# Kernel optimization log

Hardware: AMD Instinct MI355X
Metric: run time of the kernel (lower is better)

## Reference

```python
import jax, jax.numpy as jnp
import numpy as np

EPS = 1e-7
INF = 1e8
NUM_CLASSES = 80
SOFT_CENTER_RADIUS = 3.0
TOPK = 13
IOU_WEIGHT = 3.0

B, N, G, C = 16, 8400, 100, NUM_CLASSES
IMG = 640.0


def setup_inputs() -> dict:
    key = jax.random.key(0)
    ks = jax.random.split(key, 8)
    # anchor priors: centers in image, stride column (cx, cy, s, s)
    ctr = jax.random.uniform(ks[0], (N, 2)) * IMG
    stride = jnp.full((N, 1), 8.0)
    priors = jnp.concatenate([ctr, stride, stride], axis=-1)
    # predicted boxes: xyxy around random centers
    pc = jax.random.uniform(ks[1], (B, N, 2)) * IMG
    pwh = jax.random.uniform(ks[2], (B, N, 2)) * 64.0 + 8.0
    pred_bboxes = jnp.concatenate([pc - pwh / 2, pc + pwh / 2], axis=-1)
    pred_scores = jax.random.normal(ks[3], (B, N, C))
    # gt boxes: xyxy
    gc = jax.random.uniform(ks[4], (B, G, 2)) * (IMG - 40.0) + 20.0
    gwh = jax.random.uniform(ks[5], (B, G, 2)) * 128.0 + 16.0
    gt_bboxes = jnp.concatenate([gc - gwh / 2, gc + gwh / 2], axis=-1)
    gt_labels = jax.random.randint(ks[6], (B, G, 1), 0, NUM_CLASSES, dtype=jnp.int32)
    pad_bbox_flag = jnp.ones((B, G, 1), dtype=jnp.float32)
    gt_bboxes_area = gwh[..., 0] * gwh[..., 1]
    area_rule = jnp.array([0.0, 32.0, 96.0, 1.0e4], dtype=jnp.float32)
    return {
        'pred_bboxes': pred_bboxes, 'pred_scores': pred_scores, 'priors': priors,
        'gt_labels': gt_labels, 'gt_bboxes': gt_bboxes, 'pad_bbox_flag': pad_bbox_flag,
        'gt_bboxes_area': gt_bboxes_area, 'area_rule': area_rule,
    }


def _giou(b1, b2):
    # b1, b2 broadcastable [..., 4] xyxy -> GIoU [...]
    lt = jnp.maximum(b1[..., :2], b2[..., :2])
    rb = jnp.minimum(b1[..., 2:], b2[..., 2:])
    wh = jnp.clip(rb - lt, 0.0)
    overlap = wh[..., 0] * wh[..., 1]
    a1 = (b1[..., 2] - b1[..., 0]) * (b1[..., 3] - b1[..., 1])
    a2 = (b2[..., 2] - b2[..., 0]) * (b2[..., 3] - b2[..., 1])
    union = jnp.maximum(a1 + a2 - overlap, EPS)
    iou = overlap / union
    elt = jnp.minimum(b1[..., :2], b2[..., :2])
    erb = jnp.maximum(b1[..., 2:], b2[..., 2:])
    ewh = jnp.clip(erb - elt, 0.0)
    enclose = jnp.maximum(ewh[..., 0] * ewh[..., 1], EPS)
    return iou - (enclose - union) / enclose


def _forward(pred_bboxes, pred_scores, priors, gt_labels, gt_bboxes, pad_bbox_flag,
             gt_bboxes_area, area_rule):
    b, n, _ = pred_bboxes.shape
    g = gt_bboxes.shape[1]
    pts = priors[:, :2]                      # (N,2)
    # point-in-box test -> (B,N,G)
    lt = pts[None, :, None, :] - gt_bboxes[:, None, :, :2]
    rb = gt_bboxes[:, None, :, 2:] - pts[None, :, None, :]
    deltas = jnp.concatenate([lt, rb], axis=-1)          # (B,N,G,4)
    is_in = (jnp.min(deltas, axis=-1) > 0).astype(pred_bboxes.dtype)
    is_in = is_in * pad_bbox_flag[:, None, :, 0]
    # soft center prior
    gt_ctr = (gt_bboxes[..., :2] + gt_bboxes[..., 2:]) / 2.0
    strides = priors[:, 2]
    dist = jnp.sqrt(((pts[None, :, None, :] - gt_ctr[:, None, :, :]) ** 2).sum(-1))
    dist = dist / strides[None, :, None] * is_in
    soft_center_prior = jnp.power(10.0, dist - SOFT_CENTER_RADIUS) * is_in
    # pairwise GIoU (B,N,G)
    giou = _giou(pred_bboxes[:, :, None, :], gt_bboxes[:, None, :, :])
    pairwise_ious = jnp.abs(giou * is_in)
    iou_cost = -jnp.log(pairwise_ious + EPS) * IOU_WEIGHT
    # per-gt-class logit gather: (B,N,G)
    labels = gt_labels[..., 0].astype(jnp.int32)         # (B,G)
    idx = jnp.broadcast_to(labels[:, None, :], (b, n, g))
    logits = jnp.take_along_axis(pred_scores, idx, axis=2)
    sig = jax.nn.sigmoid(logits)
    scale = pairwise_ious - sig
    # stable BCE-with-logits against soft target pairwise_ious
    bce = jnp.maximum(logits, 0.0) - logits * pairwise_ious + jnp.log1p(jnp.exp(-jnp.abs(logits)))
    cls_cost = bce * jnp.exp(jnp.abs(scale) - 1.0) * jnp.abs(scale)
    cost = cls_cost + iou_cost + soft_center_prior
    in_mask = is_in > 0
    cost = jnp.where(in_mask, cost, INF)
    # dynamic-k matching
    k = min(TOPK, n)
    topk_ious = jax.lax.top_k(jnp.transpose(pairwise_ious, (0, 2, 1)), k)[0]  # (B,G,k)
    dyn_k = jnp.clip(topk_ious.sum(-1).astype(jnp.int32), 1, None)            # (B,G)
    ranks = jnp.argsort(jnp.argsort(cost, axis=1), axis=1)                    # (B,N,G)
    valid_gt = pad_bbox_flag[..., 0] > 0                                      # (B,G)
    matching = (ranks < dyn_k[:, None, :]) & valid_gt[:, None, :]             # (B,N,G)
    # resolve anchors matched to >1 gt: keep min-cost gt
    multi = matching.sum(-1) > 1                                              # (B,N)
    onehot_min = jax.nn.one_hot(jnp.argmin(cost, axis=-1), g, dtype=jnp.bool_)
    matching = jnp.where(multi[..., None], onehot_min, matching)
    fg_mask = matching.sum(-1) > 0                                            # (B,N)
    mf = matching.astype(pairwise_ious.dtype)
    matched_ious = (mf * pairwise_ious).sum(-1)                               # (B,N)
    matched_gt = jnp.argmax(mf, axis=-1)                                      # (B,N)
    # dense assignments
    assigned_labels = jnp.where(fg_mask, jnp.take_along_axis(labels, matched_gt, axis=1), NUM_CLASSES)
    gidx = jnp.broadcast_to(matched_gt[..., None], (b, n, 4))
    assigned_bboxes = jnp.where(fg_mask[..., None], jnp.take_along_axis(gt_bboxes, gidx, axis=1), 0.0)
    assign_metrics = jnp.where(fg_mask, matched_ious, 0.0)
    onehot = jax.nn.one_hot(assigned_labels, NUM_CLASSES + 1, dtype=pred_scores.dtype)[..., :NUM_CLASSES]
    assigned_scores = onehot * jnp.where(fg_mask, matched_ious, 1.0)[..., None]
    # per-class positive counts and dynamic class weights
    assigned_labels_num = (onehot * fg_mask[..., None].astype(onehot.dtype)).sum((0, 1))
    maxc = assigned_labels_num.max()
    dynamic_gt_class_weight = jnp.where(assigned_labels_num > 0,
                                        maxc / jnp.maximum(assigned_labels_num, 1.0), 1.0)
    assigned_labels_weights = jnp.where(fg_mask[..., None],
                                        dynamic_gt_class_weight[None, None, :],
                                        jnp.ones((), pred_scores.dtype))
    # gt area distribution (len(area_rule)-1, B, G)
    r2 = area_rule ** 2
    ga = gt_bboxes_area[None]
    area_dist = (ga >= r2[:-1, None, None]) & (ga < r2[1:, None, None]) & valid_gt[None]
    return (assigned_labels.astype(jnp.int32), assigned_labels_weights, assigned_bboxes,
            assigned_scores, assign_metrics, fg_mask, assigned_labels_num,
            dynamic_gt_class_weight, area_dist)


def reference(pred_bboxes, pred_scores, priors, gt_labels, gt_bboxes, pad_bbox_flag,
              gt_bboxes_area, area_rule):
    return _forward(pred_bboxes, pred_scores, priors, gt_labels, gt_bboxes,
                    pad_bbox_flag, gt_bboxes_area, area_rule)
```

## Files before the change

kernel.cpp:

```cpp
#include <hip/hip_runtime.h>

typedef unsigned long long u64;

#define BB 16
#define NN 8400
#define GG 100
#define CC 80
#define KTOP 13
#define EPSF 1e-7f
#define INFC 1e8f
#define MAXIN 1024

static constexpr size_t kO_LAB  = 0;
static constexpr size_t kO_W    = (size_t)BB * NN;
static constexpr size_t kO_BB   = kO_W + (size_t)BB * NN * CC;
static constexpr size_t kO_SC   = kO_BB + (size_t)BB * NN * 4;
static constexpr size_t kO_MET  = kO_SC + (size_t)BB * NN * CC;
static constexpr size_t kO_FG   = kO_MET + (size_t)BB * NN;
static constexpr size_t kO_NUM  = kO_FG + (size_t)BB * NN;
static constexpr size_t kO_DYNW = kO_NUM + CC;
static constexpr size_t kO_AREA = kO_DYNW + CC;

__device__ __forceinline__ unsigned f2u(float x) {
    unsigned b = __float_as_uint(x);
    return (b & 0x80000000u) ? ~b : (b | 0x80000000u);
}
__device__ __forceinline__ float u2f(unsigned e) {
    return __uint_as_float((e & 0x80000000u) ? (e & 0x7fffffffu) : ~e);
}

__device__ __forceinline__ void pair_cost_iou_inside(
    float px, float py, float st,
    float p0, float p1, float p2, float p3,
    float g0, float g1, float g2, float g3,
    float lg, float flag,
    float& cost, float& piou)
{
    float gcx = (g0 + g2) * 0.5f, gcy = (g1 + g3) * 0.5f;
    float dx = px - gcx, dy = py - gcy;
    float dist = sqrtf(dx * dx + dy * dy) / st * flag;
    float scp = exp2f((dist - 3.0f) * 3.32192809488736f) * flag;
    float ix1 = fmaxf(p0, g0), iy1 = fmaxf(p1, g1);
    float ix2 = fminf(p2, g2), iy2 = fminf(p3, g3);
    float ow = fmaxf(ix2 - ix1, 0.0f), oh = fmaxf(iy2 - iy1, 0.0f);
    float ov = ow * oh;
    float a1 = (p2 - p0) * (p3 - p1);
    float a2 = (g2 - g0) * (g3 - g1);
    float uni = fmaxf(a1 + a2 - ov, EPSF);
    float iou = ov / uni;
    float ex1 = fminf(p0, g0), ey1 = fminf(p1, g1);
    float ex2 = fmaxf(p2, g2), ey2 = fmaxf(p3, g3);
    float ew = fmaxf(ex2 - ex1, 0.0f), eh = fmaxf(ey2 - ey1, 0.0f);
    float enc = fmaxf(ew * eh, EPSF);
    float giou = iou - (enc - uni) / enc;
    piou = fabsf(giou * flag);
    float iou_cost = -__logf(piou + EPSF) * 3.0f;
    float sig = 1.0f / (1.0f + __expf(-lg));
    float sc = piou - sig;
    float asc = fabsf(sc);
    float bce = fmaxf(lg, 0.0f) - lg * piou + log1pf(__expf(-fabsf(lg)));
    float cls = bce * __expf(asc - 1.0f) * asc;
    cost = cls + iou_cost + scp;
}

__device__ __forceinline__ void pair_cost_iou(
    float px, float py, float st,
    float p0, float p1, float p2, float p3,
    float g0, float g1, float g2, float g3,
    float lg, float flag,
    float& cost, float& piou)
{
    float l = px - g0, t = py - g1, r = g2 - px, d = g3 - py;
    float mn = fminf(fminf(l, t), fminf(r, d));
    float is_in = (mn > 0.0f) ? flag : 0.0f;
    float gcx = (g0 + g2) * 0.5f, gcy = (g1 + g3) * 0.5f;
    float dx = px - gcx, dy = py - gcy;
    float dist = sqrtf(dx * dx + dy * dy) / st * is_in;
    float scp = exp2f((dist - 3.0f) * 3.32192809488736f) * is_in;
    float ix1 = fmaxf(p0, g0), iy1 = fmaxf(p1, g1);
    float ix2 = fminf(p2, g2), iy2 = fminf(p3, g3);
    float ow = fmaxf(ix2 - ix1, 0.0f), oh = fmaxf(iy2 - iy1, 0.0f);
    float ov = ow * oh;
    float a1 = (p2 - p0) * (p3 - p1);
    float a2 = (g2 - g0) * (g3 - g1);
    float uni = fmaxf(a1 + a2 - ov, EPSF);
    float iou = ov / uni;
    float ex1 = fminf(p0, g0), ey1 = fminf(p1, g1);
    float ex2 = fmaxf(p2, g2), ey2 = fmaxf(p3, g3);
    float ew = fmaxf(ex2 - ex1, 0.0f), eh = fmaxf(ey2 - ey1, 0.0f);
    float enc = fmaxf(ew * eh, EPSF);
    float giou = iou - (enc - uni) / enc;
    piou = fabsf(giou * is_in);
    float iou_cost = -__logf(piou + EPSF) * 3.0f;
    float sig = 1.0f / (1.0f + __expf(-lg));
    float sc = piou - sig;
    float asc = fabsf(sc);
    float bce = fmaxf(lg, 0.0f) - lg * piou + log1pf(__expf(-fabsf(lg)));
    float cls = bce * __expf(asc - 1.0f) * asc;
    float cc = cls + iou_cost + scp;
    cost = (is_in > 0.0f) ? cc : INFC;
}

__global__ __launch_bounds__(256) void k1_match(
    const float* __restrict__ pred_bboxes,
    const float* __restrict__ pred_scores,
    const float* __restrict__ priors,
    const int*   __restrict__ gt_labels,
    const float* __restrict__ gt_bboxes,
    const float* __restrict__ pad_flag,
    int*   __restrict__ match_count,
    int*   __restrict__ match_g,
    float* __restrict__ match_iou)
{
    __shared__ int   s_cnt;
    __shared__ int   s_list[MAXIN];
    __shared__ u64   s_cand[4 * KTOP];
    __shared__ float s_candP[4 * KTOP];
    __shared__ int   s_dynk;

    int bg = blockIdx.x;
    int b = bg / GG, g = bg - b * GG;
    int tid  = threadIdx.x;
    int lane = tid & 63;
    int w    = tid >> 6;

    float flag = pad_flag[bg];
    if (flag == 0.0f) return;

    if (tid == 0) s_cnt = 0;
    __syncthreads();

    float4 gb = *reinterpret_cast<const float4*>(gt_bboxes + (size_t)bg * 4);

    #pragma unroll 4
    for (int k = 0; k < 32; ++k) {
        int n = tid + (k << 8);
        float4 p = *reinterpret_cast<const float4*>(priors + (size_t)n * 4);
        float mn = fminf(fminf(p.x - gb.x, p.y - gb.y),
                         fminf(gb.z - p.x, gb.w - p.y));
        if (mn > 0.0f) {
            int po = atomicAdd(&s_cnt, 1);
            if (po < MAXIN) s_list[po] = n;
        }
    }
    if (tid < NN - 8192) {
        int n = tid + 8192;
        float4 p = *reinterpret_cast<const float4*>(priors + (size_t)n * 4);
        float mn = fminf(fminf(p.x - gb.x, p.y - gb.y),
                         fminf(gb.z - p.x, gb.w - p.y));
        if (mn > 0.0f) {
            int po = atomicAdd(&s_cnt, 1);
            if (po < MAXIN) s_list[po] = n;
        }
    }
    __syncthreads();
    int M = min(s_cnt, MAXIN);

    if (M == 0) {
        if (tid == 0) {
            int idx = b * NN;
            atomicAdd(&match_count[idx], 1);
            match_g[idx]   = g;
            match_iou[idx] = 0.0f;
        }
        return;
    }

    int lab = gt_labels[bg];

    u64 zs = ((u64)0x80000000u << 32) | (0x10000u + (unsigned)tid * 4u);
    u64 iK0 = zs, iK1 = zs + 1, iK2 = zs + 2, iK3 = zs + 3;
    u64 cK0 = ~0ull, cK1 = ~0ull, cK2 = ~0ull, cK3 = ~0ull;
    float cP0 = 0.f, cP1 = 0.f, cP2 = 0.f, cP3 = 0.f;

    for (int m = tid; m < M; m += 256) {
        int n = s_list[m];
        float4 pr = *reinterpret_cast<const float4*>(priors + (size_t)n * 4);
        float4 pb = *reinterpret_cast<const float4*>(pred_bboxes + ((size_t)b * NN + n) * 4);
        float lg = pred_scores[((size_t)b * NN + n) * CC + lab];
        float cost, piou;
        pair_cost_iou_inside(pr.x, pr.y, pr.z, pb.x, pb.y, pb.z, pb.w,
                             gb.x, gb.y, gb.z, gb.w, lg, flag, cost, piou);
        u64 ki = ((u64)f2u(piou) << 32) | (unsigned)n;
        if (ki > iK3) {
            iK3 = ki;
            if (iK3 > iK2) { u64 t0 = iK2; iK2 = iK3; iK3 = t0; }
            if (iK2 > iK1) { u64 t0 = iK1; iK1 = iK2; iK2 = t0; }
            if (iK1 > iK0) { u64 t0 = iK0; iK0 = iK1; iK1 = t0; }
        }
        u64 kc = ((u64)f2u(cost) << 32) | (unsigned)n;
        if (kc < cK3) {
            cK3 = kc; cP3 = piou;
            if (cK3 < cK2) { u64 t0 = cK2; cK2 = cK3; cK3 = t0; float f0 = cP2; cP2 = cP3; cP3 = f0; }
            if (cK2 < cK1) { u64 t0 = cK1; cK1 = cK2; cK2 = t0; float f0 = cP1; cP1 = cP2; cP2 = f0; }
            if (cK1 < cK0) { u64 t0 = cK0; cK0 = cK1; cK1 = t0; float f0 = cP0; cP0 = cP1; cP1 = f0; }
        }
    }

    for (int r = 0; r < KTOP; ++r) {
        u64 h = iK0;
        #pragma unroll
        for (int off = 1; off < 64; off <<= 1) {
            u64 o = __shfl_xor(h, off, 64);
            if (o > h) h = o;
        }
        if (lane == 0) s_cand[w * KTOP + r] = h;
        if (iK0 == h) { iK0 = iK1; iK1 = iK2; iK2 = iK3; iK3 = 0ull; }
    }
    __syncthreads();
    if (w == 0) {
        u64 kk = (lane < 4 * KTOP) ? s_cand[lane] : 0ull;
        float ks = 0.0f;
        for (int r = 0; r < KTOP; ++r) {
            u64 h = kk;
            #pragma unroll
            for (int off = 1; off < 64; off <<= 1) {
                u64 o = __shfl_xor(h, off, 64);
                if (o > h) h = o;
            }
            ks += u2f((unsigned)(h >> 32));
            if (kk == h) kk = 0ull;
        }
        if (lane == 0) { int dk = (int)ks; s_dynk = (dk < 1) ? 1 : dk; }
    }
    __syncthreads();
    int dyn_k = s_dynk;

    for (int r = 0; r < dyn_k; ++r) {
        u64 h = cK0;
        #pragma unroll
        for (int off = 1; off < 64; off <<= 1) {
            u64 o = __shfl_xor(h, off, 64);
            if (o < h) h = o;
        }
        if (cK0 == h) {
            s_cand[w * KTOP + r]  = h;
            s_candP[w * KTOP + r] = cP0;
            cK0 = cK1; cP0 = cP1; cK1 = cK2; cP1 = cP2; cK2 = cK3; cP2 = cP3;
            cK3 = ~0ull;
        }
    }
    __syncthreads();
    if (w == 0) {
        int tot = 4 * dyn_k;
        u64 kk = ~0ull; float pp = 0.0f;
        if (lane < tot) {
            int wv = lane / dyn_k;
            int r  = lane - wv * dyn_k;
            kk = s_cand[wv * KTOP + r];
            pp = s_candP[wv * KTOP + r];
        }
        for (int r = 0; r < dyn_k; ++r) {
            u64 h = kk;
            #pragma unroll
            for (int off = 1; off < 64; off <<= 1) {
                u64 o = __shfl_xor(h, off, 64);
                if (o < h) h = o;
            }
            if (kk == h && h != ~0ull) {
                int bi = (int)(h & 0xffffffffu);
                int idx = b * NN + bi;
                atomicAdd(&match_count[idx], 1);
                match_g[idx]   = g;
                match_iou[idx] = pp;
                kk = ~0ull;
            }
        }
    }
}

__global__ __launch_bounds__(256) void k2_resolve(
    const float* __restrict__ pred_bboxes,
    const float* __restrict__ pred_scores,
    const float* __restrict__ priors,
    const int*   __restrict__ gt_labels,
    const float* __restrict__ gt_bboxes,
    const float* __restrict__ pad_flag,
    const int*   __restrict__ match_count,
    const int*   __restrict__ match_g,
    const float* __restrict__ match_iou,
    int*   __restrict__ r_lab,
    float* __restrict__ r_miou,
    int*   __restrict__ class_num,
    float* __restrict__ out)
{
    int i = blockIdx.x * 256 + threadIdx.x;
    int lane = threadIdx.x & 63;
    int cnt = match_count[i];
    int b = i / NN;

    int lab = CC;
    float miou = 0.0f;
    float4 bbx = make_float4(0.0f, 0.0f, 0.0f, 0.0f);

    if (cnt == 1) {
        int g = match_g[i];
        int gi = b * GG + g;
        miou = match_iou[i];
        lab = gt_labels[gi];
        bbx = *reinterpret_cast<const float4*>(gt_bboxes + (size_t)gi * 4);
    }

    u64 mask = __ballot(cnt > 1);
    while (mask) {
        int src = __builtin_ctzll(mask);
        mask &= mask - 1;
        int ii = (i & ~63) | src;
        int b2 = ii / NN, n2 = ii - b2 * NN;
        float4 pr = *reinterpret_cast<const float4*>(priors + (size_t)n2 * 4);
        float4 pb = *reinterpret_cast<const float4*>(pred_bboxes + (size_t)ii * 4);
        u64 bk = ~0ull; float bp = 0.0f;
        #pragma unroll
        for (int s = 0; s < 2; ++s) {
            int gg = lane + (s << 6);
            if (gg < GG) {
                int gi = b2 * GG + gg;
                float fl = pad_flag[gi];
                float4 gbx = *reinterpret_cast<const float4*>(gt_bboxes + (size_t)gi * 4);
                int lb = gt_labels[gi];
                float lg = pred_scores[(size_t)ii * CC + lb];
                float cost, piou;
                pair_cost_iou(pr.x, pr.y, pr.z, pb.x, pb.y, pb.z, pb.w,
                              gbx.x, gbx.y, gbx.z, gbx.w, lg, fl, cost, piou);
                u64 k = ((u64)f2u(cost) << 32) | (unsigned)gg;
                if (k < bk) { bk = k; bp = piou; }
            }
        }
        #pragma unroll
        for (int off = 1; off < 64; off <<= 1) {
            u64 ok = __shfl_xor(bk, off, 64);
            float op = __shfl_xor(bp, off, 64);
            if (ok < bk) { bk = ok; bp = op; }
        }
        if (lane == src) {
            int gw = (int)(bk & 0xffffffffu);
            int gi = b2 * GG + gw;
            lab = gt_labels[gi];
            miou = bp;
            bbx = *reinterpret_cast<const float4*>(gt_bboxes + (size_t)gi * 4);
        }
    }

    bool fg = cnt > 0;
    if (fg) atomicAdd(&class_num[lab], 1);
    r_lab[i]  = lab;
    r_miou[i] = miou;
    out[kO_LAB + i] = (float)lab;
    out[kO_FG  + i] = fg ? 1.0f : 0.0f;
    out[kO_MET + i] = miou;
    *reinterpret_cast<float4*>(out + kO_BB + (size_t)i * 4) = bbx;
}

__global__ __launch_bounds__(256) void k35_weights_area(
    const int*   __restrict__ class_num,
    float* __restrict__ dynw,
    const float* __restrict__ gt_area,
    const float* __restrict__ area_rule,
    const float* __restrict__ pad_flag,
    float* __restrict__ out)
{
    if (blockIdx.x == 0) {
        int lane = threadIdx.x;
        if (lane < 64) {
            int n0 = class_num[lane];
            int n1 = (lane < CC - 64) ? class_num[lane + 64] : 0;
            int m = max(n0, n1);
            #pragma unroll
            for (int off = 32; off > 0; off >>= 1) m = max(m, __shfl_down(m, off, 64));
            m = __shfl(m, 0, 64);
            float fm = (float)m;
            {
                float wv = (n0 > 0) ? fm / fmaxf((float)n0, 1.0f) : 1.0f;
                dynw[lane] = wv;
                out[kO_NUM  + lane] = (float)n0;
                out[kO_DYNW + lane] = wv;
            }
            if (lane < CC - 64) {
                float wv = (n1 > 0) ? fm / fmaxf((float)n1, 1.0f) : 1.0f;
                dynw[lane + 64] = wv;
                out[kO_NUM  + lane + 64] = (float)n1;
                out[kO_DYNW + lane + 64] = wv;
            }
        }
    } else {
        int idx = (blockIdx.x - 1) * 256 + threadIdx.x;
        if (idx < 3 * BB * GG) {
            int z = idx / (BB * GG);
            int rem = idx - z * (BB * GG);
            float ga = gt_area[rem];
            float lo = area_rule[z] * area_rule[z];
            float hi = area_rule[z + 1] * area_rule[z + 1];
            bool v = (ga >= lo) && (ga < hi) && (pad_flag[rem] > 0.0f);
            out[kO_AREA + idx] = v ? 1.0f : 0.0f;
        }
    }
}

__global__ __launch_bounds__(256) void k4_fill(
    const int*   __restrict__ r_lab,
    const float* __restrict__ r_miou,
    const float* __restrict__ dynw,
    float* __restrict__ out)
{
    __shared__ float s_w[CC];
    if (threadIdx.x < CC) s_w[threadIdx.x] = dynw[threadIdx.x];
    __syncthreads();
    unsigned t = blockIdx.x * 256u + threadIdx.x;
    unsigned i = t / 20u;
    unsigned cq = (t - i * 20u) * 4u;
    int lab = r_lab[i];
    float miou = r_miou[i];
    bool fg = lab < CC;
    unsigned ulab = (unsigned)lab;
    float4 sc, wv;
    sc.x = (ulab == cq + 0u) ? miou : 0.0f;
    sc.y = (ulab == cq + 1u) ? miou : 0.0f;
    sc.z = (ulab == cq + 2u) ? miou : 0.0f;
    sc.w = (ulab == cq + 3u) ? miou : 0.0f;
    wv.x = fg ? s_w[cq + 0u] : 1.0f;
    wv.y = fg ? s_w[cq + 1u] : 1.0f;
    wv.z = fg ? s_w[cq + 2u] : 1.0f;
    wv.w = fg ? s_w[cq + 3u] : 1.0f;
    size_t base = (size_t)i * CC + cq;
    *reinterpret_cast<float4*>(out + kO_SC + base) = sc;
    *reinterpret_cast<float4*>(out + kO_W  + base) = wv;
}

extern "C" void kernel_launch(void* const* d_in, const int* in_sizes, int n_in,
                              void* d_out, int out_size, void* d_ws, size_t ws_size,
                              hipStream_t stream)
{
    const float* pred_bboxes = (const float*)d_in[0];
    const float* pred_scores = (const float*)d_in[1];
    const float* priors      = (const float*)d_in[2];
    const int*   gt_labels   = (const int*)d_in[3];
    const float* gt_bboxes   = (const float*)d_in[4];
    const float* pad_flag    = (const float*)d_in[5];
    const float* gt_area     = (const float*)d_in[6];
    const float* area_rule   = (const float*)d_in[7];
    float* out = (float*)d_out;

    char* w = (char*)d_ws;
    int*   match_count = (int*)w;   w += (size_t)BB * NN * 4;
    int*   class_num   = (int*)w;   w += (size_t)CC * 4;
    int*   match_g     = (int*)w;   w += (size_t)BB * NN * 4;
    float* match_iou   = (float*)w; w += (size_t)BB * NN * 4;
    int*   r_lab       = (int*)w;   w += (size_t)BB * NN * 4;
    float* r_miou      = (float*)w; w += (size_t)BB * NN * 4;
    float* dynw        = (float*)w; w += (size_t)CC * 4;

    hipMemsetAsync(d_ws, 0, (size_t)(BB * NN + CC) * 4, stream);

    k1_match<<<BB * GG, 256, 0, stream>>>(
        pred_bboxes, pred_scores, priors, gt_labels, gt_bboxes, pad_flag,
        match_count, match_g, match_iou);

    k2_resolve<<<BB * NN / 256, 256, 0, stream>>>(
        pred_bboxes, pred_scores, priors, gt_labels, gt_bboxes, pad_flag,
        match_count, match_g, match_iou, r_lab, r_miou, class_num, out);

    k35_weights_area<<<1 + (3 * BB * GG + 255) / 256, 256, 0, stream>>>(
        class_num, dynw, gt_area, area_rule, pad_flag, out);

    k4_fill<<<(int)((size_t)BB * NN * (CC / 4) / 256), 256, 0, stream>>>(
        r_lab, r_miou, dynw, out);
}
```

Measured before the change: 232.2 us.

## Replace per-thread top-k lists with shared-memory rank counting; fuse weight kernel into fill

The matching kernel no longer keeps per-thread top-4 registers merged by wavefront shuffle reductions. It stores the iou and cost keys for every candidate in shared memory and computes each candidate's rank by an O(M^2) comparison scan. That rank then gives the top-13 IoU sum and the dynamic-k selection without serial shuffle rounds. The separate class-weight/area kernel is folded into the fill kernel, with every block recomputing the 80 class weights, which removes one launch and the dynw round trip. The risks are quadratic shared-memory work when M is large and larger shared-memory use (about 18KB) lowering occupancy.

```diff
diff --git a/kernel.cpp b/kernel.cpp
--- a/kernel.cpp
+++ b/kernel.cpp
@@ -114,20 +114,20 @@
 {
     __shared__ int   s_cnt;
     __shared__ int   s_list[MAXIN];
-    __shared__ u64   s_cand[4 * KTOP];
-    __shared__ float s_candP[4 * KTOP];
-    __shared__ int   s_dynk;
+    __shared__ u64   s_kiou[MAXIN];
+    __shared__ u64   s_kcost[MAXIN];
+    __shared__ unsigned short s_rc[MAXIN];
+    __shared__ float s_top[KTOP];
 
     int bg = blockIdx.x;
     int b = bg / GG, g = bg - b * GG;
-    int tid  = threadIdx.x;
-    int lane = tid & 63;
-    int w    = tid >> 6;
+    int tid = threadIdx.x;
 
     float flag = pad_flag[bg];
     if (flag == 0.0f) return;
 
     if (tid == 0) s_cnt = 0;
+    if (tid < KTOP) s_top[tid] = 0.0f;
     __syncthreads();
 
     float4 gb = *reinterpret_cast<const float4*>(gt_bboxes + (size_t)bg * 4);
@@ -168,11 +168,6 @@
 
     int lab = gt_labels[bg];
 
-    u64 zs = ((u64)0x80000000u << 32) | (0x10000u + (unsigned)tid * 4u);
-    u64 iK0 = zs, iK1 = zs + 1, iK2 = zs + 2, iK3 = zs + 3;
-    u64 cK0 = ~0ull, cK1 = ~0ull, cK2 = ~0ull, cK3 = ~0ull;
-    float cP0 = 0.f, cP1 = 0.f, cP2 = 0.f, cP3 = 0.f;
-
     for (int m = tid; m < M; m += 256) {
         int n = s_list[m];
         float4 pr = *reinterpret_cast<const float4*>(priors + (size_t)n * 4);
@@ -181,90 +176,39 @@
         float cost, piou;
         pair_cost_iou_inside(pr.x, pr.y, pr.z, pb.x, pb.y, pb.z, pb.w,
                              gb.x, gb.y, gb.z, gb.w, lg, flag, cost, piou);
-        u64 ki = ((u64)f2u(piou) << 32) | (unsigned)n;
-        if (ki > iK3) {
-            iK3 = ki;
-            if (iK3 > iK2) { u64 t0 = iK2; iK2 = iK3; iK3 = t0; }
-            if (iK2 > iK1) { u64 t0 = iK1; iK1 = iK2; iK2 = t0; }
-            if (iK1 > iK0) { u64 t0 = iK0; iK0 = iK1; iK1 = t0; }
-        }
-        u64 kc = ((u64)f2u(cost) << 32) | (unsigned)n;
-        if (kc < cK3) {
-            cK3 = kc; cP3 = piou;
-            if (cK3 < cK2) { u64 t0 = cK2; cK2 = cK3; cK3 = t0; float f0 = cP2; cP2 = cP3; cP3 = f0; }
-            if (cK2 < cK1) { u64 t0 = cK1; cK1 = cK2; cK2 = t0; float f0 = cP1; cP1 = cP2; cP2 = f0; }
-            if (cK1 < cK0) { u64 t0 = cK0; cK0 = cK1; cK1 = t0; float f0 = cP0; cP0 = cP1; cP1 = f0; }
-        }
-    }
-
-    for (int r = 0; r < KTOP; ++r) {
-        u64 h = iK0;
-        #pragma unroll
-        for (int off = 1; off < 64; off <<= 1) {
-            u64 o = __shfl_xor(h, off, 64);
-            if (o > h) h = o;
-        }
-        if (lane == 0) s_cand[w * KTOP + r] = h;
-        if (iK0 == h) { iK0 = iK1; iK1 = iK2; iK2 = iK3; iK3 = 0ull; }
-    }
-    __syncthreads();
-    if (w == 0) {
-        u64 kk = (lane < 4 * KTOP) ? s_cand[lane] : 0ull;
-        float ks = 0.0f;
-        for (int r = 0; r < KTOP; ++r) {
-            u64 h = kk;
-            #pragma unroll
-            for (int off = 1; off < 64; off <<= 1) {
-                u64 o = __shfl_xor(h, off, 64);
-                if (o > h) h = o;
-            }
-            ks += u2f((unsigned)(h >> 32));
-            if (kk == h) kk = 0ull;
-        }
-        if (lane == 0) { int dk = (int)ks; s_dynk = (dk < 1) ? 1 : dk; }
-    }
-    __syncthreads();
-    int dyn_k = s_dynk;
-
-    for (int r = 0; r < dyn_k; ++r) {
-        u64 h = cK0;
-        #pragma unroll
-        for (int off = 1; off < 64; off <<= 1) {
-            u64 o = __shfl_xor(h, off, 64);
-            if (o < h) h = o;
-        }
-        if (cK0 == h) {
-            s_cand[w * KTOP + r]  = h;
-            s_candP[w * KTOP + r] = cP0;
-            cK0 = cK1; cP0 = cP1; cK1 = cK2; cP1 = cP2; cK2 = cK3; cP2 = cP3;
-            cK3 = ~0ull;
-        }
-    }
-    __syncthreads();
-    if (w == 0) {
-        int tot = 4 * dyn_k;
-        u64 kk = ~0ull; float pp = 0.0f;
-        if (lane < tot) {
-            int wv = lane / dyn_k;
-            int r  = lane - wv * dyn_k;
-            kk = s_cand[wv * KTOP + r];
-            pp = s_candP[wv * KTOP + r];
-        }
-        for (int r = 0; r < dyn_k; ++r) {
-            u64 h = kk;
-            #pragma unroll
-            for (int off = 1; off < 64; off <<= 1) {
-                u64 o = __shfl_xor(h, off, 64);
-                if (o < h) h = o;
-            }
-            if (kk == h && h != ~0ull) {
-                int bi = (int)(h & 0xffffffffu);
-                int idx = b * NN + bi;
-                atomicAdd(&match_count[idx], 1);
-                match_g[idx]   = g;
-                match_iou[idx] = pp;
-                kk = ~0ull;
-            }
+        s_kiou[m]  = ((u64)f2u(piou) << 32) | (unsigned)n;
+        s_kcost[m] = ((u64)f2u(cost) << 32) | (unsigned)n;
+    }
+    __syncthreads();
+
+    for (int m = tid; m < M; m += 256) {
+        u64 ki = s_kiou[m];
+        u64 kc = s_kcost[m];
+        int riou = 0, rcost = 0;
+        #pragma unroll 4
+        for (int i = 0; i < M; ++i) {
+            riou  += (s_kiou[i]  > ki) ? 1 : 0;
+            rcost += (s_kcost[i] < kc) ? 1 : 0;
+        }
+        if (riou < KTOP) s_top[riou] = u2f((unsigned)(ki >> 32));
+        s_rc[m] = (unsigned short)rcost;
+    }
+    __syncthreads();
+
+    float ksum = 0.0f;
+    #pragma unroll
+    for (int r = 0; r < KTOP; ++r) ksum += s_top[r];
+    int dyn_k = (int)ksum;
+    if (dyn_k < 1) dyn_k = 1;
+
+    for (int m = tid; m < M; m += 256) {
+        if ((int)s_rc[m] < dyn_k) {
+            u64 ki = s_kiou[m];
+            int n = (int)(ki & 0xffffffffu);
+            int idx = b * NN + n;
+            atomicAdd(&match_count[idx], 1);
+            match_g[idx]   = g;
+            match_iou[idx] = u2f((unsigned)(ki >> 32));
         }
     }
 }
@@ -351,39 +295,55 @@
     *reinterpret_cast<float4*>(out + kO_BB + (size_t)i * 4) = bbx;
 }
 
-__global__ __launch_bounds__(256) void k35_weights_area(
+#define K4MAIN ((BB * NN * (CC / 4)) / 256)
+__global__ __launch_bounds__(256) void k4_fill(
+    const int*   __restrict__ r_lab,
+    const float* __restrict__ r_miou,
     const int*   __restrict__ class_num,
-    float* __restrict__ dynw,
     const float* __restrict__ gt_area,
     const float* __restrict__ area_rule,
     const float* __restrict__ pad_flag,
     float* __restrict__ out)
 {
-    if (blockIdx.x == 0) {
-        int lane = threadIdx.x;
-        if (lane < 64) {
-            int n0 = class_num[lane];
-            int n1 = (lane < CC - 64) ? class_num[lane + 64] : 0;
-            int m = max(n0, n1);
-            #pragma unroll
-            for (int off = 32; off > 0; off >>= 1) m = max(m, __shfl_down(m, off, 64));
-            m = __shfl(m, 0, 64);
-            float fm = (float)m;
-            {
-                float wv = (n0 > 0) ? fm / fmaxf((float)n0, 1.0f) : 1.0f;
-                dynw[lane] = wv;
-                out[kO_NUM  + lane] = (float)n0;
-                out[kO_DYNW + lane] = wv;
-            }
-            if (lane < CC - 64) {
-                float wv = (n1 > 0) ? fm / fmaxf((float)n1, 1.0f) : 1.0f;
-                dynw[lane + 64] = wv;
-                out[kO_NUM  + lane + 64] = (float)n1;
-                out[kO_DYNW + lane + 64] = wv;
-            }
-        }
+    __shared__ float s_w[CC];
+    int t0 = threadIdx.x;
+    if (t0 < 64) {
+        int n0 = class_num[t0];
+        int n1 = (t0 < CC - 64) ? class_num[t0 + 64] : 0;
+        int m = max(n0, n1);
+        #pragma unroll
+        for (int off = 32; off > 0; off >>= 1) m = max(m, __shfl_down(m, off, 64));
+        m = __shfl(m, 0, 64);
+        float fm = (float)m;
+        s_w[t0] = (n0 > 0) ? fm / fmaxf((float)n0, 1.0f) : 1.0f;
+        if (t0 < CC - 64)
+            s_w[t0 + 64] = (n1 > 0) ? fm / fmaxf((float)n1, 1.0f) : 1.0f;
+    }
+    __syncthreads();
+
+    unsigned bid = blockIdx.x;
+    if (bid < K4MAIN) {
+        unsigned t = bid * 256u + threadIdx.x;
+        unsigned i = t / 20u;
+        unsigned cq = (t - i * 20u) * 4u;
+        int lab = r_lab[i];
+        float miou = r_miou[i];
+        bool fg = lab < CC;
+        unsigned ulab = (unsigned)lab;
+        float4 sc, wv;
+        sc.x = (ulab == cq + 0u) ? miou : 0.0f;
+        sc.y = (ulab == cq + 1u) ? miou : 0.0f;
+        sc.z = (ulab == cq + 2u) ? miou : 0.0f;
+        sc.w = (ulab == cq + 3u) ? miou : 0.0f;
+        wv.x = fg ? s_w[cq + 0u] : 1.0f;
+        wv.y = fg ? s_w[cq + 1u] : 1.0f;
+        wv.z = fg ? s_w[cq + 2u] : 1.0f;
+        wv.w = fg ? s_w[cq + 3u] : 1.0f;
+        size_t base = (size_t)i * CC + cq;
+        *reinterpret_cast<float4*>(out + kO_SC + base) = sc;
+        *reinterpret_cast<float4*>(out + kO_W  + base) = wv;
     } else {
-        int idx = (blockIdx.x - 1) * 256 + threadIdx.x;
+        int idx = (int)(bid - K4MAIN) * 256 + threadIdx.x;
         if (idx < 3 * BB * GG) {
             int z = idx / (BB * GG);
             int rem = idx - z * (BB * GG);
@@ -392,38 +352,14 @@
             float hi = area_rule[z + 1] * area_rule[z + 1];
             bool v = (ga >= lo) && (ga < hi) && (pad_flag[rem] > 0.0f);
             out[kO_AREA + idx] = v ? 1.0f : 0.0f;
-        }
-    }
-}
-
-__global__ __launch_bounds__(256) void k4_fill(
-    const int*   __restrict__ r_lab,
-    const float* __restrict__ r_miou,
-    const float* __restrict__ dynw,
-    float* __restrict__ out)
-{
-    __shared__ float s_w[CC];
-    if (threadIdx.x < CC) s_w[threadIdx.x] = dynw[threadIdx.x];
-    __syncthreads();
-    unsigned t = blockIdx.x * 256u + threadIdx.x;
-    unsigned i = t / 20u;
-    unsigned cq = (t - i * 20u) * 4u;
-    int lab = r_lab[i];
-    float miou = r_miou[i];
-    bool fg = lab < CC;
-    unsigned ulab = (unsigned)lab;
-    float4 sc, wv;
-    sc.x = (ulab == cq + 0u) ? miou : 0.0f;
-    sc.y = (ulab == cq + 1u) ? miou : 0.0f;
-    sc.z = (ulab == cq + 2u) ? miou : 0.0f;
-    sc.w = (ulab == cq + 3u) ? miou : 0.0f;
-    wv.x = fg ? s_w[cq + 0u] : 1.0f;
-    wv.y = fg ? s_w[cq + 1u] : 1.0f;
-    wv.z = fg ? s_w[cq + 2u] : 1.0f;
-    wv.w = fg ? s_w[cq + 3u] : 1.0f;
-    size_t base = (size_t)i * CC + cq;
-    *reinterpret_cast<float4*>(out + kO_SC + base) = sc;
-    *reinterpret_cast<float4*>(out + kO_W  + base) = wv;
+        } else if (idx < 3 * BB * GG + CC) {
+            int c = idx - 3 * BB * GG;
+            out[kO_NUM + c] = (float)class_num[c];
+        } else if (idx < 3 * BB * GG + 2 * CC) {
+            int c = idx - 3 * BB * GG - CC;
+            out[kO_DYNW + c] = s_w[c];
+        }
+    }
 }
 
 extern "C" void kernel_launch(void* const* d_in, const int* in_sizes, int n_in,
@@ -447,7 +383,6 @@
     float* match_iou   = (float*)w; w += (size_t)BB * NN * 4;
     int*   r_lab       = (int*)w;   w += (size_t)BB * NN * 4;
     float* r_miou      = (float*)w; w += (size_t)BB * NN * 4;
-    float* dynw        = (float*)w; w += (size_t)CC * 4;
 
     hipMemsetAsync(d_ws, 0, (size_t)(BB * NN + CC) * 4, stream);
 
@@ -459,9 +394,6 @@
         pred_bboxes, pred_scores, priors, gt_labels, gt_bboxes, pad_flag,
         match_count, match_g, match_iou, r_lab, r_miou, class_num, out);
 
-    k35_weights_area<<<1 + (3 * BB * GG + 255) / 256, 256, 0, stream>>>(
-        class_num, dynw, gt_area, area_rule, pad_flag, out);
-
-    k4_fill<<<(int)((size_t)BB * NN * (CC / 4) / 256), 256, 0, stream>>>(
-        r_lab, r_miou, dynw, out);
-}
+    k4_fill<<<K4MAIN + (3 * BB * GG + 2 * CC + 255) / 256, 256, 0, stream>>>(
+        r_lab, r_miou, class_num, gt_area, area_rule, pad_flag, out);
+}
```

After: 223.3 us. -3.8%, faster.
